# Optimization experiments

Measured on AMD Instinct MI355X. Metric: run time of the kernel, lower is better.

## Reference

```python
import jax, jax.numpy as jnp
import numpy as np
from jax.scipy.linalg import expm

S = 64          # alphabet size (codons)
M = 8           # number of models, prod(model_shape)
N_LEAVES = 32   # leaves of the balanced binary tree
N_EDGES = 62    # nodes 0..62, every non-root node has one parent edge (edge id == child node id)
B = 1024        # batch (alignment columns)
# per-level ranges of child-node ids; node 32+j has children (2j, 2j+1), etc.
LEVELS = [(0, 32), (32, 48), (48, 56), (56, 60), (60, 62)]


def inv_stereographic_projection(p):
    # maps R^{s-1} -> unit sphere S^{s-1}
    n2 = jnp.sum(p * p, axis=-1, keepdims=True)
    return jnp.concatenate([2.0 * p / (n2 + 1.0), (n2 - 1.0) / (n2 + 1.0)], axis=-1)


def generator(R, pi):
    # R: (M, s(s-1)/2) exchangeabilities, pi: (M, s) stationary distribution
    iu, ju = np.triu_indices(S, 1)
    A = jnp.zeros((M, S, S), R.dtype).at[:, iu, ju].set(R).at[:, ju, iu].set(R)
    Q = A * pi[:, None, :]                       # Q_ij = A_ij * pi_j (off-diagonal)
    row = jnp.sum(Q, axis=-1)                    # (M, S)
    return Q - jnp.eye(S, dtype=Q.dtype) * row[:, :, None]


def felsenstein(leave_configuration, R_inv, pi_inv, lengths):
    pi = inv_stereographic_projection(pi_inv) ** 2           # (M, S), rows sum to 1
    R = jnp.exp(R_inv)                                       # positive rates
    Q = generator(R, pi)                                     # (M, S, S)
    tQ = lengths[:, None, None, None] * Q[None]              # (E, M, S, S)
    P = jax.vmap(expm)(tQ.reshape(-1, S, S)).reshape(N_EDGES, M, S, S)
    # leaf alphas: tile leaf observations over the M models -> (n_leaves, B, M, S)
    prev = jnp.broadcast_to(
        leave_configuration.transpose(1, 0, 2)[:, :, None, :],
        (N_LEAVES, leave_configuration.shape[0], M, S))
    # level-synchronous pruning: messages up each parent edge, then product of the two children
    for a, b in LEVELS:
        msg = jnp.einsum('emcd,ebmd->ebmc', P[a:b], prev)    # per-edge transition
        prev = msg[0::2] * msg[1::2]                         # combine sibling pairs
    root = prev[0]                                           # (B, M, S)
    out = jnp.einsum('bms,ms->bm', root, pi)                 # P(data | model m)
    return out.reshape(out.shape[0], M)                      # (B, *model_shape)


def setup_inputs() -> dict:
    key = jax.random.key(0)
    k1, k2, k3, k4 = jax.random.split(key, 4)
    leave_configuration = jax.random.uniform(k1, (B, N_LEAVES, S), dtype=jnp.float32)
    tree_indices = jnp.zeros((B,), dtype=jnp.int32)          # single tree (F=1)
    R_inv = jax.random.uniform(k2, (M, S * (S - 1) // 2), dtype=jnp.float32,
                               minval=-1.0, maxval=1.0)
    pi_inv = jnp.full((M, S - 1), 1.0 / (np.sqrt(S) - 1.0), dtype=jnp.float32) \
        + 0.01 * jax.random.normal(k3, (M, S - 1), dtype=jnp.float32)
    lengths = jax.random.uniform(k4, (N_EDGES,), dtype=jnp.float32,
                                 minval=0.05, maxval=0.5)
    return {'leave_configuration': leave_configuration, 'R_inv': R_inv,
            'pi_inv': pi_inv, 'lengths': lengths, 'tree_indices': tree_indices}


def reference(leave_configuration, R_inv, pi_inv, lengths, tree_indices):
    # F=1: tf.dynamic_partition/gather_nd batch slicing is the identity, so
    # tree_indices is closed over / unused.
    return felsenstein(leave_configuration, R_inv, pi_inv, lengths)
```

## Files before the change

kernel.cpp:

```cpp
#include <hip/hip_runtime.h>

typedef unsigned short u16;
typedef unsigned int u32;
typedef __attribute__((ext_vector_type(8))) __bf16 bf16x8;
typedef __attribute__((ext_vector_type(4))) float f32x4;

constexpr size_t OFF_PI  = 0;
constexpr size_t OFF_PBH = 512;
constexpr size_t OFF_PBL = OFF_PBH + 1015808;

union FR { uint4 u; bf16x8 v; };

__device__ __forceinline__ void split_bf16(float x, u16& h, u16& l) {
  u32 b = __float_as_uint(x);
  u32 hb = (b + 0x7fffu + ((b >> 16) & 1u)) & 0xffff0000u;
  h = (u16)(hb >> 16);
  float r = x - __uint_as_float(hb);
  l = (u16)(__float_as_uint(r) >> 16);
}

__device__ __forceinline__ void split8(const f32x4 a, const f32x4 b,
                                       uint4& hi, uint4& lo) {
  u16 h[8], l[8];
  split_bf16(a.x, h[0], l[0]); split_bf16(a.y, h[1], l[1]);
  split_bf16(a.z, h[2], l[2]); split_bf16(a.w, h[3], l[3]);
  split_bf16(b.x, h[4], l[4]); split_bf16(b.y, h[5], l[5]);
  split_bf16(b.z, h[6], l[6]); split_bf16(b.w, h[7], l[7]);
  hi.x = h[0] | ((u32)h[1] << 16); hi.y = h[2] | ((u32)h[3] << 16);
  hi.z = h[4] | ((u32)h[5] << 16); hi.w = h[6] | ((u32)h[7] << 16);
  lo.x = l[0] | ((u32)l[1] << 16); lo.y = l[2] | ((u32)l[3] << 16);
  lo.z = l[4] | ((u32)l[5] << 16); lo.w = l[6] | ((u32)l[7] << 16);
}

__device__ __forceinline__ void mfma3(f32x4& a, const uint4 ah, const uint4 al,
                                      const uint4 bh, const uint4 bl) {
  FR Ah, Al, Bh, Bl;
  Ah.u = ah; Al.u = al; Bh.u = bh; Bl.u = bl;
  a = __builtin_amdgcn_mfma_f32_16x16x32_bf16(Ah.v, Bh.v, a, 0, 0, 0);
  a = __builtin_amdgcn_mfma_f32_16x16x32_bf16(Ah.v, Bl.v, a, 0, 0, 0);
  a = __builtin_amdgcn_mfma_f32_16x16x32_bf16(Al.v, Bh.v, a, 0, 0, 0);
}

__device__ __forceinline__ void xt_read2(const u32* b, int row, int chunk,
                                         uint4& hi, uint4& lo) {
  const int dw = (row << 5) + (((chunk + row) & 7) << 2);
  hi = *(const uint4*)&b[dw];
  lo = *(const uint4*)&b[2048 + dw];
}
__device__ __forceinline__ void xt_write4(u32* b, int row, int cp, int half,
                                          const f32x4 v) {
  u16 h[4], l[4];
  split_bf16(v.x, h[0], l[0]); split_bf16(v.y, h[1], l[1]);
  split_bf16(v.z, h[2], l[2]); split_bf16(v.w, h[3], l[3]);
  const int dw = (row << 5) + (((cp + row) & 7) << 2) + half * 2;
  uint2 hh, ll;
  hh.x = h[0] | ((u32)h[1] << 16); hh.y = h[2] | ((u32)h[3] << 16);
  ll.x = l[0] | ((u32)l[1] << 16); ll.y = l[2] | ((u32)l[3] << 16);
  *(uint2*)&b[dw] = hh;
  *(uint2*)&b[2048 + dw] = ll;
}

__global__ __launch_bounds__(512, 2) void k_pcomb(
    const float* __restrict__ R_inv, const float* __restrict__ pi_inv,
    const float* __restrict__ lengths, float* __restrict__ ws,
    u16* __restrict__ PBH, u16* __restrict__ PBL) {
  const int m = blockIdx.x & 7, prt = blockIdx.x >> 3;
  const int tid = threadIdx.x, lane = tid & 63, w = tid >> 6;
  const int ln = lane & 15, kq = lane >> 4;
  __shared__ float pis[64];
  __shared__ float n2s;
  __shared__ __align__(16) float Qs[64 * 68];
  __shared__ __align__(16) u32 PB[8][4096];

  if (tid < 64) {
    float p = (tid < 63) ? pi_inv[m * 63 + tid] : 0.f;
    float v = p * p;
    #pragma unroll
    for (int off = 32; off; off >>= 1) v += __shfl_down(v, off, 64);
    if (tid == 0) n2s = v;
  }
  __syncthreads();
  if (tid < 64) {
    const float den = n2s + 1.f;
    const float x = (tid < 63) ? 2.f * pi_inv[m * 63 + tid] / den
                               : (n2s - 1.f) / den;
    const float pv = x * x;
    pis[tid] = pv;
    if (prt == 0) ws[OFF_PI + (size_t)m * 64 + tid] = pv;
  }
  __syncthreads();
  for (int idx = tid; idx < 4096; idx += 512) {
    const int i = idx >> 6, j = idx & 63;
    float q = 0.f;
    if (i != j) {
      const int a = min(i, j), b = max(i, j);
      const int kk = a * (127 - a) / 2 + (b - a - 1);
      q = expf(R_inv[m * 2016 + kk]) * pis[j];
    }
    Qs[i * 68 + j] = q;
  }
  __syncthreads();
  if (tid < 64) {
    float s = 0.f;
    #pragma unroll 4
    for (int j4 = 0; j4 < 64; j4 += 4) {
      const f32x4 q = *(const f32x4*)&Qs[tid * 68 + j4];
      s += q.x + q.y + q.z + q.w;
    }
    Qs[tid * 68 + tid] = -s;
  }
  __syncthreads();

  float q[12][2][4];
  #pragma unroll
  for (int tt = 0; tt < 2; ++tt) {
    const int T = w + tt * 8, ct = T >> 2, bt = T & 3;
    #pragma unroll
    for (int r = 0; r < 4; ++r)
      q[0][tt][r] = Qs[(ct * 16 + kq * 4 + r) * 68 + bt * 16 + ln];
  }
  {
    const int i = tid >> 3, c = tid & 7;
    const f32x4 a = *(const f32x4*)&Qs[i * 68 + c * 8];
    const f32x4 b = *(const f32x4*)&Qs[i * 68 + c * 8 + 4];
    uint4 h, l;
    split8(a, b, h, l);
    const int dw = (i << 5) + (((c + i) & 7) << 2);
    *(uint4*)&PB[0][dw] = h;
    *(uint4*)&PB[0][2048 + dw] = l;
    const int j = i;
    f32x4 ca, cb;
    ca.x = Qs[(c * 8 + 0) * 68 + j]; ca.y = Qs[(c * 8 + 1) * 68 + j];
    ca.z = Qs[(c * 8 + 2) * 68 + j]; ca.w = Qs[(c * 8 + 3) * 68 + j];
    cb.x = Qs[(c * 8 + 4) * 68 + j]; cb.y = Qs[(c * 8 + 5) * 68 + j];
    cb.z = Qs[(c * 8 + 6) * 68 + j]; cb.w = Qs[(c * 8 + 7) * 68 + j];
    split8(ca, cb, h, l);
    *(uint4*)&PB[4][dw] = h;
    *(uint4*)&PB[4][2048 + dw] = l;
  }
  __syncthreads();

  const f32x4 z = {0.f, 0.f, 0.f, 0.f};
  auto tileP = [&](const u32* RX, const u32* CY, int T) -> f32x4 {
    const int ct = T >> 2, bt = T & 3;
    uint4 ah[2], al[2], bh[2], bl[2];
    #pragma unroll
    for (int kh = 0; kh < 2; ++kh) {
      xt_read2(RX, ct * 16 + ln, kh * 4 + kq, ah[kh], al[kh]);
      xt_read2(CY, bt * 16 + ln, kh * 4 + kq, bh[kh], bl[kh]);
    }
    f32x4 a = z;
    #pragma unroll
    for (int kh = 0; kh < 2; ++kh) mfma3(a, ah[kh], al[kh], bh[kh], bl[kh]);
    return a;
  };
  auto tileT = [&](const u32* RX, const u32* CY, int T) -> f32x4 {
    const int ct = T >> 2, bt = T & 3;
    uint4 ah[2], al[2], bh[2], bl[2];
    #pragma unroll
    for (int kh = 0; kh < 2; ++kh) {
      xt_read2(CY, ct * 16 + ln, kh * 4 + kq, ah[kh], al[kh]);
      xt_read2(RX, bt * 16 + ln, kh * 4 + kq, bh[kh], bl[kh]);
    }
    f32x4 a = z;
    #pragma unroll
    for (int kh = 0; kh < 2; ++kh) mfma3(a, ah[kh], al[kh], bh[kh], bl[kh]);
    return a;
  };
  auto wbuf = [&](u32* dst, int T, const f32x4 a) {
    const int ct = T >> 2, bt = T & 3;
    xt_write4(dst, bt * 16 + ln, 2 * ct + (kq >> 1), kq & 1, a);
  };

  #pragma unroll
  for (int tt = 0; tt < 2; ++tt) {
    const int T = w + tt * 8;
    const f32x4 a = tileP(PB[0], PB[4], T);
    #pragma unroll
    for (int r = 0; r < 4; ++r) q[1][tt][r] = a[r];
    wbuf(PB[5], T, a);
    wbuf(PB[1], T, tileT(PB[0], PB[4], T));
  }
  __syncthreads();
  #pragma unroll
  for (int tt = 0; tt < 2; ++tt) {
    const int T = w + tt * 8;
    const f32x4 a3 = tileP(PB[1], PB[4], T);
    const f32x4 a4 = tileP(PB[1], PB[5], T);
    #pragma unroll
    for (int r = 0; r < 4; ++r) { q[2][tt][r] = a3[r]; q[3][tt][r] = a4[r]; }
    wbuf(PB[6], T, a3);
    wbuf(PB[7], T, a4);
    wbuf(PB[2], T, tileT(PB[1], PB[5], T));
  }
  __syncthreads();
  #pragma unroll
  for (int tt = 0; tt < 2; ++tt) {
    const int T = w + tt * 8;
    const f32x4 a5 = tileP(PB[2], PB[4], T);
    const f32x4 a6 = tileP(PB[2], PB[5], T);
    const f32x4 a7 = tileP(PB[2], PB[6], T);
    const f32x4 a8 = tileP(PB[2], PB[7], T);
    #pragma unroll
    for (int r = 0; r < 4; ++r) {
      q[4][tt][r] = a5[r]; q[5][tt][r] = a6[r];
      q[6][tt][r] = a7[r]; q[7][tt][r] = a8[r];
    }
    wbuf(PB[3], T, tileT(PB[2], PB[7], T));
  }
  __syncthreads();
  #pragma unroll
  for (int tt = 0; tt < 2; ++tt) {
    const int T = w + tt * 8;
    const f32x4 a9  = tileP(PB[3], PB[4], T);
    const f32x4 a10 = tileP(PB[3], PB[5], T);
    const f32x4 a11 = tileP(PB[3], PB[6], T);
    const f32x4 a12 = tileP(PB[3], PB[7], T);
    #pragma unroll
    for (int r = 0; r < 4; ++r) {
      q[8][tt][r] = a9[r];  q[9][tt][r] = a10[r];
      q[10][tt][r] = a11[r]; q[11][tt][r] = a12[r];
    }
  }

  #pragma unroll
  for (int ei = 0; ei < 2; ++ei) {
    const int e = prt * 2 + ei;
    if (e >= 62) break;
    const float t = lengths[e];
    const size_t base = ((size_t)e * 8 + m) << 12;
    #pragma unroll
    for (int tt = 0; tt < 2; ++tt) {
      const int T = w + tt * 8, ct = T >> 2, bt = T & 3;
      float av[4];
      #pragma unroll
      for (int r = 0; r < 4; ++r)
        av[r] = (ct == bt && ln == kq * 4 + r) ? 1.f : 0.f;
      float cf = 1.f;
      #pragma unroll
      for (int k = 1; k <= 12; ++k) {
        cf *= t / (float)k;
        #pragma unroll
        for (int r = 0; r < 4; ++r) av[r] = fmaf(cf, q[k - 1][tt][r], av[r]);
      }
      #pragma unroll
      for (int r = 0; r < 4; ++r) {
        u16 h, l;
        split_bf16(av[r], h, l);
        const size_t off =
            base + (size_t)(ct * 16 + kq * 4 + r) * 64 + bt * 16 + ln;
        PBH[off] = h;
        PBL[off] = l;
      }
    }
  }
}

__global__ __launch_bounds__(512, 2) void k_tree(
    const float* __restrict__ leaves, const u16* __restrict__ Phi,
    const u16* __restrict__ Plo, const float* __restrict__ ws,
    float* __restrict__ out) {
  const int m = blockIdx.x & 7, btile = blockIdx.x >> 3;
  const int tid = threadIdx.x, lane = tid & 63, w = tid >> 6;
  const int ln = lane & 15, kq = lane >> 4;
  __shared__ __align__(16) u32 slots[16 * 2048];
  __shared__ float psum[2][4][16];
  const f32x4 z = {0.f, 0.f, 0.f, 0.f};

  auto node_read = [&](int slot, int row, int kh, uint4& bh, uint4& bl) {
    const int jc = kh * 8 + kq * 2;
    const u32* b = &slots[slot * 2048 + row * 64];
    const uint4 A = *(const uint4*)&b[((jc + row) & 15) << 2];
    const uint4 B = *(const uint4*)&b[((jc + 1 + row) & 15) << 2];
    bh.x = A.x; bh.y = A.y; bh.z = B.x; bh.w = B.y;
    bl.x = A.z; bl.y = A.w; bl.z = B.z; bl.w = B.w;
  };
  auto node_write = [&](int slot, int row, int jc, const f32x4 v) {
    u16 h[4], l[4];
    split_bf16(v.x, h[0], l[0]); split_bf16(v.y, h[1], l[1]);
    split_bf16(v.z, h[2], l[2]); split_bf16(v.w, h[3], l[3]);
    uint4 pk;
    pk.x = h[0] | ((u32)h[1] << 16); pk.y = h[2] | ((u32)h[3] << 16);
    pk.z = l[0] | ((u32)l[1] << 16); pk.w = l[2] | ((u32)l[3] << 16);
    *(uint4*)&slots[slot * 2048 + row * 64 + (((jc + row) & 15) << 2)] = pk;
  };

  auto do_pair = [&](int eb, int p, int s0, int s1, int outSlot, int bt0,
                     int nbt, int ct0, int nct, bool leaf, f32x4* rootout) {
    uint4 bfh[2][2][2], bfl[2][2][2];
    #pragma unroll
    for (int s = 0; s < 2; ++s)
      #pragma unroll
      for (int bi = 0; bi < 2; ++bi) {
        if (bi >= nbt) continue;
        const int row = (bt0 + bi) * 16 + ln;
        #pragma unroll
        for (int kh = 0; kh < 2; ++kh) {
          if (leaf) {
            const float* g = leaves + (size_t)(btile * 32 + row) * 2048 +
                             (size_t)(eb + 2 * p + s) * 64 + kh * 32 + kq * 8;
            const f32x4 xa = *(const f32x4*)g;
            const f32x4 xb = *(const f32x4*)(g + 4);
            split8(xa, xb, bfh[s][bi][kh], bfl[s][bi][kh]);
          } else {
            node_read(s ? s1 : s0, row, kh, bfh[s][bi][kh], bfl[s][bi][kh]);
          }
        }
      }
    uint4 ph[2][4][2], pl[2][4][2];
    #pragma unroll
    for (int s = 0; s < 2; ++s) {
      const size_t pb = ((size_t)(eb + 2 * p + s) * 8 + m) << 12;
      #pragma unroll
      for (int ci = 0; ci < 4; ++ci) {
        if (ci >= nct) continue;
        #pragma unroll
        for (int kh = 0; kh < 2; ++kh) {
          const size_t off =
              pb + (size_t)((ct0 + ci) * 16 + ln) * 64 + kh * 32 + kq * 8;
          ph[s][ci][kh] = *(const uint4*)(Phi + off);
          pl[s][ci][kh] = *(const uint4*)(Plo + off);
        }
      }
    }
    f32x4 a0[4][2];
    #pragma unroll
    for (int ci = 0; ci < 4; ++ci) {
      if (ci >= nct) continue;
      #pragma unroll
      for (int bi = 0; bi < 2; ++bi) {
        if (bi >= nbt) continue;
        f32x4 a = z;
        #pragma unroll
        for (int kh = 0; kh < 2; ++kh)
          mfma3(a, ph[0][ci][kh], pl[0][ci][kh], bfh[0][bi][kh], bfl[0][bi][kh]);
        a0[ci][bi] = a;
      }
    }
    #pragma unroll
    for (int ci = 0; ci < 4; ++ci) {
      if (ci >= nct) continue;
      #pragma unroll
      for (int bi = 0; bi < 2; ++bi) {
        if (bi >= nbt) continue;
        f32x4 a = z;
        #pragma unroll
        for (int kh = 0; kh < 2; ++kh)
          mfma3(a, ph[1][ci][kh], pl[1][ci][kh], bfh[1][bi][kh], bfl[1][bi][kh]);
        const f32x4 pr = a0[ci][bi] * a;
        if (rootout)
          *rootout = pr;
        else
          node_write(outSlot, (bt0 + bi) * 16 + ln, (ct0 + ci) * 4 + kq, pr);
      }
    }
  };

  do_pair(0, w, -1, -1, w, 0, 2, 0, 4, true, nullptr);
  do_pair(0, w + 8, -1, -1, w + 8, 0, 2, 0, 4, true, nullptr);
  __syncthreads();
  do_pair(32, w, 2 * w, 2 * w + 1, 2 * w, 0, 2, 0, 4, false, nullptr);
  __syncthreads();
  {
    const int j = w >> 1, bi = w & 1;
    do_pair(48, j, 4 * j, 4 * j + 2, 4 * j, bi, 1, 0, 4, false, nullptr);
  }
  __syncthreads();
  {
    const int j = w >> 2, bi = w & 1, ch = (w >> 1) & 1;
    do_pair(56, j, 8 * j, 8 * j + 4, 8 * j + 1, bi, 1, ch * 2, 2, false,
            nullptr);
  }
  __syncthreads();
  {
    f32x4 pr = z;
    do_pair(60, 0, 1, 9, -1, w & 1, 1, w >> 1, 1, false, &pr);
    const f32x4 piv =
        *(const f32x4*)&ws[OFF_PI + (size_t)m * 64 + (w >> 1) * 16 + kq * 4];
    float v = pr.x * piv.x + pr.y * piv.y + pr.z * piv.z + pr.w * piv.w;
    v += __shfl_xor(v, 16, 64);
    v += __shfl_xor(v, 32, 64);
    if (lane < 16) psum[w & 1][w >> 1][lane] = v;
  }
  __syncthreads();
  if (tid < 32) {
    const int bi = tid >> 4, bb = tid & 15;
    out[(size_t)(btile * 32 + tid) * 8 + m] =
        psum[bi][0][bb] + psum[bi][1][bb] + psum[bi][2][bb] + psum[bi][3][bb];
  }
}

extern "C" void kernel_launch(void* const* d_in, const int* in_sizes, int n_in,
                              void* d_out, int out_size, void* d_ws, size_t ws_size,
                              hipStream_t stream) {
  const float* leaves  = (const float*)d_in[0];
  const float* R_inv   = (const float*)d_in[1];
  const float* pi_inv  = (const float*)d_in[2];
  const float* lengths = (const float*)d_in[3];
  float* out = (float*)d_out;
  float* ws  = (float*)d_ws;

  u16* PBH = (u16*)(ws + OFF_PBH);
  u16* PBL = (u16*)(ws + OFF_PBL);

  hipLaunchKernelGGL(k_pcomb, dim3(256), dim3(512), 0, stream, R_inv, pi_inv,
                     lengths, ws, PBH, PBL);
  hipLaunchKernelGGL(k_tree, dim3(256), dim3(512), 0, stream, leaves, PBH, PBL,
                     ws, out);
}
```

Baseline: 119.8 us.

## Replace level-synchronous tree kernel with single-wave depth-first register recursion

The shared-memory, 8-wave level-synchronous pruning kernel is replaced by a template-recursive depth-first evaluation run by one 64-thread wave per (16-column tile, model). Intermediate node vectors stay in registers and are reshaped into MFMA B-operand layout with cross-lane shuffles instead of LDS round trips, which removes all __syncthreads and LDS traffic. The trade-off is a much smaller block size with only 512 single-wave blocks, heavier register pressure and code size from full unrolling, serial depth-first execution inside each wave, and P-matrix reloads per 16-column tile instead of per 32-column tile.

```diff
diff --git a/kernel.cpp b/kernel.cpp
--- a/kernel.cpp
+++ b/kernel.cpp
@@ -256,138 +256,140 @@
   }
 }
 
-__global__ __launch_bounds__(512, 2) void k_tree(
+struct NV { uint2 H[4]; uint2 L[4]; };
+
+struct Ctx {
+  const float* leaves;
+  const u16* Phi;
+  const u16* Plo;
+  int ln, kq, m;
+  size_t colbase;
+};
+
+__device__ __forceinline__ void leafB(const Ctx& c, int leaf, uint4 bh[2],
+                                      uint4 bl[2]) {
+  #pragma unroll
+  for (int kh = 0; kh < 2; ++kh) {
+    const float* g = c.leaves + (c.colbase + c.ln) * 2048 +
+                     (size_t)leaf * 64 + kh * 32 + c.kq * 8;
+    const f32x4 xa = *(const f32x4*)g;
+    const f32x4 xb = *(const f32x4*)(g + 4);
+    split8(xa, xb, bh[kh], bl[kh]);
+  }
+}
+
+__device__ __forceinline__ void nvB(const Ctx& c, const NV& v, uint4 bh[2],
+                                    uint4 bl[2]) {
+  const int A = c.ln + ((c.kq & 1) << 5);
+  const int B = A + 16;
+  const bool hiCt = (c.kq & 2) != 0;
+  #pragma unroll
+  for (int kh = 0; kh < 2; ++kh) {
+    const uint2 h0 = v.H[kh * 2], h1 = v.H[kh * 2 + 1];
+    const uint2 l0 = v.L[kh * 2], l1 = v.L[kh * 2 + 1];
+    const u32 hxA0 = __shfl((int)h0.x, A, 64), hyA0 = __shfl((int)h0.y, A, 64);
+    const u32 hxB0 = __shfl((int)h0.x, B, 64), hyB0 = __shfl((int)h0.y, B, 64);
+    const u32 hxA1 = __shfl((int)h1.x, A, 64), hyA1 = __shfl((int)h1.y, A, 64);
+    const u32 hxB1 = __shfl((int)h1.x, B, 64), hyB1 = __shfl((int)h1.y, B, 64);
+    bh[kh].x = hiCt ? hxA1 : hxA0; bh[kh].y = hiCt ? hyA1 : hyA0;
+    bh[kh].z = hiCt ? hxB1 : hxB0; bh[kh].w = hiCt ? hyB1 : hyB0;
+    const u32 lxA0 = __shfl((int)l0.x, A, 64), lyA0 = __shfl((int)l0.y, A, 64);
+    const u32 lxB0 = __shfl((int)l0.x, B, 64), lyB0 = __shfl((int)l0.y, B, 64);
+    const u32 lxA1 = __shfl((int)l1.x, A, 64), lyA1 = __shfl((int)l1.y, A, 64);
+    const u32 lxB1 = __shfl((int)l1.x, B, 64), lyB1 = __shfl((int)l1.y, B, 64);
+    bl[kh].x = hiCt ? lxA1 : lxA0; bl[kh].y = hiCt ? lyA1 : lyA0;
+    bl[kh].z = hiCt ? lxB1 : lxB0; bl[kh].w = hiCt ? lyB1 : lyB0;
+  }
+}
+
+__device__ __forceinline__ void edgeMsg(const Ctx& c, int e, const uint4 bh[2],
+                                        const uint4 bl[2], f32x4 mo[4]) {
+  const f32x4 z = {0.f, 0.f, 0.f, 0.f};
+  uint4 ph[4][2], pl[4][2];
+  const size_t pb = ((size_t)(e * 8 + c.m)) << 12;
+  #pragma unroll
+  for (int ci = 0; ci < 4; ++ci)
+    #pragma unroll
+    for (int kh = 0; kh < 2; ++kh) {
+      const size_t off = pb + (size_t)(ci * 16 + c.ln) * 64 + kh * 32 + c.kq * 8;
+      ph[ci][kh] = *(const uint4*)(c.Phi + off);
+      pl[ci][kh] = *(const uint4*)(c.Plo + off);
+    }
+  #pragma unroll
+  for (int ci = 0; ci < 4; ++ci) {
+    f32x4 a = z;
+    #pragma unroll
+    for (int kh = 0; kh < 2; ++kh)
+      mfma3(a, ph[ci][kh], pl[ci][kh], bh[kh], bl[kh]);
+    mo[ci] = a;
+  }
+}
+
+template <int N> __device__ __forceinline__ NV evalN(const Ctx& c);
+
+template <int C>
+__device__ __forceinline__ void childB(const Ctx& c, uint4 bh[2], uint4 bl[2]) {
+  if constexpr (C < 32) {
+    leafB(c, C, bh, bl);
+  } else {
+    const NV v = evalN<C>(c);
+    nvB(c, v, bh, bl);
+  }
+}
+
+template <int N>
+__device__ __forceinline__ NV evalN(const Ctx& c) {
+  constexpr int c0 = 2 * (N - 32);
+  uint4 b0h[2], b0l[2], b1h[2], b1l[2];
+  childB<c0>(c, b0h, b0l);
+  childB<c0 + 1>(c, b1h, b1l);
+  f32x4 m0[4], m1[4];
+  edgeMsg(c, c0, b0h, b0l, m0);
+  edgeMsg(c, c0 + 1, b1h, b1l, m1);
+  NV out;
+  #pragma unroll
+  for (int ci = 0; ci < 4; ++ci) {
+    const f32x4 pr = m0[ci] * m1[ci];
+    u16 h[4], l[4];
+    split_bf16(pr.x, h[0], l[0]); split_bf16(pr.y, h[1], l[1]);
+    split_bf16(pr.z, h[2], l[2]); split_bf16(pr.w, h[3], l[3]);
+    out.H[ci].x = h[0] | ((u32)h[1] << 16);
+    out.H[ci].y = h[2] | ((u32)h[3] << 16);
+    out.L[ci].x = l[0] | ((u32)l[1] << 16);
+    out.L[ci].y = l[2] | ((u32)l[3] << 16);
+  }
+  return out;
+}
+
+__global__ __launch_bounds__(64, 1) void k_treedf(
     const float* __restrict__ leaves, const u16* __restrict__ Phi,
     const u16* __restrict__ Plo, const float* __restrict__ ws,
     float* __restrict__ out) {
-  const int m = blockIdx.x & 7, btile = blockIdx.x >> 3;
-  const int tid = threadIdx.x, lane = tid & 63, w = tid >> 6;
-  const int ln = lane & 15, kq = lane >> 4;
-  __shared__ __align__(16) u32 slots[16 * 2048];
-  __shared__ float psum[2][4][16];
-  const f32x4 z = {0.f, 0.f, 0.f, 0.f};
-
-  auto node_read = [&](int slot, int row, int kh, uint4& bh, uint4& bl) {
-    const int jc = kh * 8 + kq * 2;
-    const u32* b = &slots[slot * 2048 + row * 64];
-    const uint4 A = *(const uint4*)&b[((jc + row) & 15) << 2];
-    const uint4 B = *(const uint4*)&b[((jc + 1 + row) & 15) << 2];
-    bh.x = A.x; bh.y = A.y; bh.z = B.x; bh.w = B.y;
-    bl.x = A.z; bl.y = A.w; bl.z = B.z; bl.w = B.w;
-  };
-  auto node_write = [&](int slot, int row, int jc, const f32x4 v) {
-    u16 h[4], l[4];
-    split_bf16(v.x, h[0], l[0]); split_bf16(v.y, h[1], l[1]);
-    split_bf16(v.z, h[2], l[2]); split_bf16(v.w, h[3], l[3]);
-    uint4 pk;
-    pk.x = h[0] | ((u32)h[1] << 16); pk.y = h[2] | ((u32)h[3] << 16);
-    pk.z = l[0] | ((u32)l[1] << 16); pk.w = l[2] | ((u32)l[3] << 16);
-    *(uint4*)&slots[slot * 2048 + row * 64 + (((jc + row) & 15) << 2)] = pk;
-  };
-
-  auto do_pair = [&](int eb, int p, int s0, int s1, int outSlot, int bt0,
-                     int nbt, int ct0, int nct, bool leaf, f32x4* rootout) {
-    uint4 bfh[2][2][2], bfl[2][2][2];
-    #pragma unroll
-    for (int s = 0; s < 2; ++s)
-      #pragma unroll
-      for (int bi = 0; bi < 2; ++bi) {
-        if (bi >= nbt) continue;
-        const int row = (bt0 + bi) * 16 + ln;
-        #pragma unroll
-        for (int kh = 0; kh < 2; ++kh) {
-          if (leaf) {
-            const float* g = leaves + (size_t)(btile * 32 + row) * 2048 +
-                             (size_t)(eb + 2 * p + s) * 64 + kh * 32 + kq * 8;
-            const f32x4 xa = *(const f32x4*)g;
-            const f32x4 xb = *(const f32x4*)(g + 4);
-            split8(xa, xb, bfh[s][bi][kh], bfl[s][bi][kh]);
-          } else {
-            node_read(s ? s1 : s0, row, kh, bfh[s][bi][kh], bfl[s][bi][kh]);
-          }
-        }
-      }
-    uint4 ph[2][4][2], pl[2][4][2];
-    #pragma unroll
-    for (int s = 0; s < 2; ++s) {
-      const size_t pb = ((size_t)(eb + 2 * p + s) * 8 + m) << 12;
-      #pragma unroll
-      for (int ci = 0; ci < 4; ++ci) {
-        if (ci >= nct) continue;
-        #pragma unroll
-        for (int kh = 0; kh < 2; ++kh) {
-          const size_t off =
-              pb + (size_t)((ct0 + ci) * 16 + ln) * 64 + kh * 32 + kq * 8;
-          ph[s][ci][kh] = *(const uint4*)(Phi + off);
-          pl[s][ci][kh] = *(const uint4*)(Plo + off);
-        }
-      }
-    }
-    f32x4 a0[4][2];
-    #pragma unroll
-    for (int ci = 0; ci < 4; ++ci) {
-      if (ci >= nct) continue;
-      #pragma unroll
-      for (int bi = 0; bi < 2; ++bi) {
-        if (bi >= nbt) continue;
-        f32x4 a = z;
-        #pragma unroll
-        for (int kh = 0; kh < 2; ++kh)
-          mfma3(a, ph[0][ci][kh], pl[0][ci][kh], bfh[0][bi][kh], bfl[0][bi][kh]);
-        a0[ci][bi] = a;
-      }
-    }
-    #pragma unroll
-    for (int ci = 0; ci < 4; ++ci) {
-      if (ci >= nct) continue;
-      #pragma unroll
-      for (int bi = 0; bi < 2; ++bi) {
-        if (bi >= nbt) continue;
-        f32x4 a = z;
-        #pragma unroll
-        for (int kh = 0; kh < 2; ++kh)
-          mfma3(a, ph[1][ci][kh], pl[1][ci][kh], bfh[1][bi][kh], bfl[1][bi][kh]);
-        const f32x4 pr = a0[ci][bi] * a;
-        if (rootout)
-          *rootout = pr;
-        else
-          node_write(outSlot, (bt0 + bi) * 16 + ln, (ct0 + ci) * 4 + kq, pr);
-      }
-    }
-  };
-
-  do_pair(0, w, -1, -1, w, 0, 2, 0, 4, true, nullptr);
-  do_pair(0, w + 8, -1, -1, w + 8, 0, 2, 0, 4, true, nullptr);
-  __syncthreads();
-  do_pair(32, w, 2 * w, 2 * w + 1, 2 * w, 0, 2, 0, 4, false, nullptr);
-  __syncthreads();
-  {
-    const int j = w >> 1, bi = w & 1;
-    do_pair(48, j, 4 * j, 4 * j + 2, 4 * j, bi, 1, 0, 4, false, nullptr);
-  }
-  __syncthreads();
-  {
-    const int j = w >> 2, bi = w & 1, ch = (w >> 1) & 1;
-    do_pair(56, j, 8 * j, 8 * j + 4, 8 * j + 1, bi, 1, ch * 2, 2, false,
-            nullptr);
-  }
-  __syncthreads();
-  {
-    f32x4 pr = z;
-    do_pair(60, 0, 1, 9, -1, w & 1, 1, w >> 1, 1, false, &pr);
+  const int m = blockIdx.x & 7, ctile = blockIdx.x >> 3;
+  const int lane = threadIdx.x & 63;
+  Ctx c;
+  c.leaves = leaves; c.Phi = Phi; c.Plo = Plo;
+  c.ln = lane & 15; c.kq = lane >> 4; c.m = m;
+  c.colbase = (size_t)ctile * 16;
+
+  uint4 b0h[2], b0l[2], b1h[2], b1l[2];
+  childB<60>(c, b0h, b0l);
+  childB<61>(c, b1h, b1l);
+  f32x4 m0[4], m1[4];
+  edgeMsg(c, 60, b0h, b0l, m0);
+  edgeMsg(c, 61, b1h, b1l, m1);
+
+  float v = 0.f;
+  #pragma unroll
+  for (int ci = 0; ci < 4; ++ci) {
+    const f32x4 pr = m0[ci] * m1[ci];
     const f32x4 piv =
-        *(const f32x4*)&ws[OFF_PI + (size_t)m * 64 + (w >> 1) * 16 + kq * 4];
-    float v = pr.x * piv.x + pr.y * piv.y + pr.z * piv.z + pr.w * piv.w;
-    v += __shfl_xor(v, 16, 64);
-    v += __shfl_xor(v, 32, 64);
-    if (lane < 16) psum[w & 1][w >> 1][lane] = v;
-  }
-  __syncthreads();
-  if (tid < 32) {
-    const int bi = tid >> 4, bb = tid & 15;
-    out[(size_t)(btile * 32 + tid) * 8 + m] =
-        psum[bi][0][bb] + psum[bi][1][bb] + psum[bi][2][bb] + psum[bi][3][bb];
-  }
+        *(const f32x4*)&ws[OFF_PI + (size_t)m * 64 + ci * 16 + c.kq * 4];
+    v += pr.x * piv.x + pr.y * piv.y + pr.z * piv.z + pr.w * piv.w;
+  }
+  v += __shfl_xor(v, 16, 64);
+  v += __shfl_xor(v, 32, 64);
+  if (lane < 16) out[(c.colbase + c.ln) * 8 + m] = v;
 }
 
 extern "C" void kernel_launch(void* const* d_in, const int* in_sizes, int n_in,
@@ -405,6 +407,6 @@
 
   hipLaunchKernelGGL(k_pcomb, dim3(256), dim3(512), 0, stream, R_inv, pi_inv,
                      lengths, ws, PBH, PBL);
-  hipLaunchKernelGGL(k_tree, dim3(256), dim3(512), 0, stream, leaves, PBH, PBL,
+  hipLaunchKernelGGL(k_treedf, dim3(512), dim3(64), 0, stream, leaves, PBH, PBL,
                      ws, out);
 }
```

Measured after the change: 283.8 us. 137% more time.

## Split tree kernel into two launches to raise block parallelism for lower levels

Applied to the files above, without the earlier changes.

Splits the tree pruning into k_treeA, which handles the leaves through level 2 across 1024 blocks (four subtrees per batch tile and model) and writes the level-2 node messages to workspace, and k_treeB, which finishes the top two levels and the root reduction. This is meant to fill the GPU with more blocks during the heavy leaf levels, with smaller shared memory per block, instead of 256 blocks each walking the whole tree. In exchange it adds a global-memory round trip for the intermediate messages and an extra kernel launch. It falls back to the old single kernel if the workspace is too small.

```diff
diff --git a/kernel.cpp b/kernel.cpp
--- a/kernel.cpp
+++ b/kernel.cpp
@@ -8,6 +8,8 @@
 constexpr size_t OFF_PI  = 0;
 constexpr size_t OFF_PBH = 512;
 constexpr size_t OFF_PBL = OFF_PBH + 1015808;
+constexpr size_t OFF_NB2 = OFF_PBL + 1015808;
+constexpr size_t NB2_FLOATS = 2097152;
 
 union FR { uint4 u; bf16x8 v; };
 
@@ -58,6 +60,21 @@
   ll.x = l[0] | ((u32)l[1] << 16); ll.y = l[2] | ((u32)l[3] << 16);
   *(uint2*)&b[dw] = hh;
   *(uint2*)&b[2048 + dw] = ll;
+}
+
+__device__ __forceinline__ uint4 pack_hl(const f32x4 v) {
+  u16 h[4], l[4];
+  split_bf16(v.x, h[0], l[0]); split_bf16(v.y, h[1], l[1]);
+  split_bf16(v.z, h[2], l[2]); split_bf16(v.w, h[3], l[3]);
+  uint4 pk;
+  pk.x = h[0] | ((u32)h[1] << 16); pk.y = h[2] | ((u32)h[3] << 16);
+  pk.z = l[0] | ((u32)l[1] << 16); pk.w = l[2] | ((u32)l[3] << 16);
+  return pk;
+}
+__device__ __forceinline__ void unpack_hl(const uint4 A, const uint4 B,
+                                          uint4& bh, uint4& bl) {
+  bh.x = A.x; bh.y = A.y; bh.z = B.x; bh.w = B.y;
+  bl.x = A.z; bl.y = A.w; bl.z = B.z; bl.w = B.w;
 }
 
 __global__ __launch_bounds__(512, 2) void k_pcomb(
@@ -272,17 +289,11 @@
     const u32* b = &slots[slot * 2048 + row * 64];
     const uint4 A = *(const uint4*)&b[((jc + row) & 15) << 2];
     const uint4 B = *(const uint4*)&b[((jc + 1 + row) & 15) << 2];
-    bh.x = A.x; bh.y = A.y; bh.z = B.x; bh.w = B.y;
-    bl.x = A.z; bl.y = A.w; bl.z = B.z; bl.w = B.w;
+    unpack_hl(A, B, bh, bl);
   };
   auto node_write = [&](int slot, int row, int jc, const f32x4 v) {
-    u16 h[4], l[4];
-    split_bf16(v.x, h[0], l[0]); split_bf16(v.y, h[1], l[1]);
-    split_bf16(v.z, h[2], l[2]); split_bf16(v.w, h[3], l[3]);
-    uint4 pk;
-    pk.x = h[0] | ((u32)h[1] << 16); pk.y = h[2] | ((u32)h[3] << 16);
-    pk.z = l[0] | ((u32)l[1] << 16); pk.w = l[2] | ((u32)l[3] << 16);
-    *(uint4*)&slots[slot * 2048 + row * 64 + (((jc + row) & 15) << 2)] = pk;
+    *(uint4*)&slots[slot * 2048 + row * 64 + (((jc + row) & 15) << 2)] =
+        pack_hl(v);
   };
 
   auto do_pair = [&](int eb, int p, int s0, int s1, int outSlot, int bt0,
@@ -390,6 +401,217 @@
   }
 }
 
+__global__ __launch_bounds__(512, 2) void k_treeA(
+    const float* __restrict__ leaves, const u16* __restrict__ Phi,
+    const u16* __restrict__ Plo, float* __restrict__ ws) {
+  const int m = blockIdx.x & 7;
+  const int q = (blockIdx.x >> 3) & 3;
+  const int btile = blockIdx.x >> 5;
+  const int tid = threadIdx.x, lane = tid & 63, w = tid >> 6;
+  const int ln = lane & 15, kq = lane >> 4;
+  __shared__ __align__(16) u32 slots[6 * 2048];
+  uint4* NB2 = (uint4*)(ws + OFF_NB2);
+  const f32x4 z = {0.f, 0.f, 0.f, 0.f};
+
+  auto slot_read = [&](int slot, int row, int kh, uint4& bh, uint4& bl) {
+    const int jc = kh * 8 + kq * 2;
+    const u32* b = &slots[slot * 2048 + row * 64];
+    const uint4 A = *(const uint4*)&b[((jc + row) & 15) << 2];
+    const uint4 B = *(const uint4*)&b[((jc + 1 + row) & 15) << 2];
+    unpack_hl(A, B, bh, bl);
+  };
+  auto slot_write = [&](int slot, int row, int jc, const f32x4 v) {
+    *(uint4*)&slots[slot * 2048 + row * 64 + (((jc + row) & 15) << 2)] =
+        pack_hl(v);
+  };
+  auto nb2_write = [&](int nidx, int row, int jc, const f32x4 v) {
+    NB2[(((size_t)(nidx * 8 + m) * 32 + btile) * 32 + row) * 16 +
+        ((jc + row) & 15)] = pack_hl(v);
+  };
+  auto edge_msg = [&](int e, const uint4 bh[2], const uint4 bl[2], int ct0,
+                      int nct, f32x4* mo) {
+    const size_t pb = ((size_t)(e * 8 + m)) << 12;
+    uint4 ph[4][2], pl[4][2];
+    #pragma unroll
+    for (int ci = 0; ci < 4; ++ci) {
+      if (ci >= nct) continue;
+      #pragma unroll
+      for (int kh = 0; kh < 2; ++kh) {
+        const size_t off =
+            pb + (size_t)((ct0 + ci) * 16 + ln) * 64 + kh * 32 + kq * 8;
+        ph[ci][kh] = *(const uint4*)(Phi + off);
+        pl[ci][kh] = *(const uint4*)(Plo + off);
+      }
+    }
+    #pragma unroll
+    for (int ci = 0; ci < 4; ++ci) {
+      if (ci >= nct) continue;
+      f32x4 a = z;
+      #pragma unroll
+      for (int kh = 0; kh < 2; ++kh)
+        mfma3(a, ph[ci][kh], pl[ci][kh], bh[kh], bl[kh]);
+      mo[ci] = a;
+    }
+  };
+
+  {
+    const int ch = w & 1, p = w >> 1;
+    const int row = ch * 16 + ln;
+    const int e0 = 8 * q + 2 * p, e1 = e0 + 1;
+    uint4 bh[2][2], bl[2][2];
+    #pragma unroll
+    for (int s = 0; s < 2; ++s)
+      #pragma unroll
+      for (int kh = 0; kh < 2; ++kh) {
+        const float* g = leaves + (size_t)(btile * 32 + row) * 2048 +
+                         (size_t)(s ? e1 : e0) * 64 + kh * 32 + kq * 8;
+        split8(*(const f32x4*)g, *(const f32x4*)(g + 4), bh[s][kh], bl[s][kh]);
+      }
+    f32x4 m0[4], m1[4];
+    edge_msg(e0, bh[0], bl[0], 0, 4, m0);
+    edge_msg(e1, bh[1], bl[1], 0, 4, m1);
+    #pragma unroll
+    for (int ci = 0; ci < 4; ++ci)
+      slot_write(p, row, ci * 4 + kq, m0[ci] * m1[ci]);
+  }
+  __syncthreads();
+  {
+    const int r = w >> 2, ch = (w >> 1) & 1, q2 = w & 1;
+    const int row = ch * 16 + ln, ct0 = 2 * q2;
+    const int e0 = 32 + 4 * q + 2 * r, e1 = e0 + 1;
+    uint4 bh[2][2], bl[2][2];
+    #pragma unroll
+    for (int s = 0; s < 2; ++s)
+      #pragma unroll
+      for (int kh = 0; kh < 2; ++kh)
+        slot_read(2 * r + s, row, kh, bh[s][kh], bl[s][kh]);
+    f32x4 m0[4], m1[4];
+    edge_msg(e0, bh[0], bl[0], ct0, 2, m0);
+    edge_msg(e1, bh[1], bl[1], ct0, 2, m1);
+    #pragma unroll
+    for (int ci = 0; ci < 2; ++ci)
+      slot_write(4 + r, row, (ct0 + ci) * 4 + kq, m0[ci] * m1[ci]);
+  }
+  __syncthreads();
+  {
+    const int ch = w & 1, cq = w >> 1;
+    const int row = ch * 16 + ln;
+    const int e0 = 48 + 2 * q, e1 = e0 + 1;
+    uint4 bh[2][2], bl[2][2];
+    #pragma unroll
+    for (int s = 0; s < 2; ++s)
+      #pragma unroll
+      for (int kh = 0; kh < 2; ++kh)
+        slot_read(4 + s, row, kh, bh[s][kh], bl[s][kh]);
+    f32x4 m0[4], m1[4];
+    edge_msg(e0, bh[0], bl[0], cq, 1, m0);
+    edge_msg(e1, bh[1], bl[1], cq, 1, m1);
+    nb2_write(q, row, cq * 4 + kq, m0[0] * m1[0]);
+  }
+}
+
+__global__ __launch_bounds__(512, 2) void k_treeB(
+    const u16* __restrict__ Phi, const u16* __restrict__ Plo,
+    const float* __restrict__ ws, float* __restrict__ out) {
+  const int m = blockIdx.x & 7, btile = blockIdx.x >> 3;
+  const int tid = threadIdx.x, lane = tid & 63, w = tid >> 6;
+  const int ln = lane & 15, kq = lane >> 4;
+  __shared__ __align__(16) u32 slots[2 * 2048];
+  __shared__ float psum[2][4][16];
+  const uint4* NB2 = (const uint4*)(ws + OFF_NB2);
+  const f32x4 z = {0.f, 0.f, 0.f, 0.f};
+
+  auto slot_read = [&](int slot, int row, int kh, uint4& bh, uint4& bl) {
+    const int jc = kh * 8 + kq * 2;
+    const u32* b = &slots[slot * 2048 + row * 64];
+    const uint4 A = *(const uint4*)&b[((jc + row) & 15) << 2];
+    const uint4 B = *(const uint4*)&b[((jc + 1 + row) & 15) << 2];
+    unpack_hl(A, B, bh, bl);
+  };
+  auto slot_write = [&](int slot, int row, int jc, const f32x4 v) {
+    *(uint4*)&slots[slot * 2048 + row * 64 + (((jc + row) & 15) << 2)] =
+        pack_hl(v);
+  };
+  auto nb2_read = [&](int nidx, int row, int kh, uint4& bh, uint4& bl) {
+    const int jc = kh * 8 + kq * 2;
+    const uint4* b =
+        NB2 + (((size_t)(nidx * 8 + m) * 32 + btile) * 32 + row) * 16;
+    const uint4 A = b[(jc + row) & 15];
+    const uint4 B = b[(jc + 1 + row) & 15];
+    unpack_hl(A, B, bh, bl);
+  };
+  auto edge_msg = [&](int e, const uint4 bh[2], const uint4 bl[2], int ct0,
+                      int nct, f32x4* mo) {
+    const size_t pb = ((size_t)(e * 8 + m)) << 12;
+    uint4 ph[4][2], pl[4][2];
+    #pragma unroll
+    for (int ci = 0; ci < 4; ++ci) {
+      if (ci >= nct) continue;
+      #pragma unroll
+      for (int kh = 0; kh < 2; ++kh) {
+        const size_t off =
+            pb + (size_t)((ct0 + ci) * 16 + ln) * 64 + kh * 32 + kq * 8;
+        ph[ci][kh] = *(const uint4*)(Phi + off);
+        pl[ci][kh] = *(const uint4*)(Plo + off);
+      }
+    }
+    #pragma unroll
+    for (int ci = 0; ci < 4; ++ci) {
+      if (ci >= nct) continue;
+      f32x4 a = z;
+      #pragma unroll
+      for (int kh = 0; kh < 2; ++kh)
+        mfma3(a, ph[ci][kh], pl[ci][kh], bh[kh], bl[kh]);
+      mo[ci] = a;
+    }
+  };
+
+  {
+    const int r = w >> 2, ch = (w >> 1) & 1, q2 = w & 1;
+    const int row = ch * 16 + ln, ct0 = 2 * q2;
+    const int e0 = 56 + 2 * r, e1 = e0 + 1;
+    uint4 bh[2][2], bl[2][2];
+    #pragma unroll
+    for (int s = 0; s < 2; ++s)
+      #pragma unroll
+      for (int kh = 0; kh < 2; ++kh)
+        nb2_read(2 * r + s, row, kh, bh[s][kh], bl[s][kh]);
+    f32x4 m0[4], m1[4];
+    edge_msg(e0, bh[0], bl[0], ct0, 2, m0);
+    edge_msg(e1, bh[1], bl[1], ct0, 2, m1);
+    #pragma unroll
+    for (int ci = 0; ci < 2; ++ci)
+      slot_write(r, row, (ct0 + ci) * 4 + kq, m0[ci] * m1[ci]);
+  }
+  __syncthreads();
+  {
+    const int ch = w & 1, cq = w >> 1;
+    const int row = ch * 16 + ln;
+    uint4 bh[2][2], bl[2][2];
+    #pragma unroll
+    for (int s = 0; s < 2; ++s)
+      #pragma unroll
+      for (int kh = 0; kh < 2; ++kh)
+        slot_read(s, row, kh, bh[s][kh], bl[s][kh]);
+    f32x4 m0[4], m1[4];
+    edge_msg(60, bh[0], bl[0], cq, 1, m0);
+    edge_msg(61, bh[1], bl[1], cq, 1, m1);
+    const f32x4 pr = m0[0] * m1[0];
+    const f32x4 piv =
+        *(const f32x4*)&ws[OFF_PI + (size_t)m * 64 + cq * 16 + kq * 4];
+    float v = pr.x * piv.x + pr.y * piv.y + pr.z * piv.z + pr.w * piv.w;
+    v += __shfl_xor(v, 16, 64);
+    v += __shfl_xor(v, 32, 64);
+    if (lane < 16) psum[ch][cq][lane] = v;
+  }
+  __syncthreads();
+  if (tid < 32) {
+    const int ch = tid >> 4, bb = tid & 15;
+    out[(size_t)(btile * 32 + tid) * 8 + m] =
+        psum[ch][0][bb] + psum[ch][1][bb] + psum[ch][2][bb] + psum[ch][3][bb];
+  }
+}
+
 extern "C" void kernel_launch(void* const* d_in, const int* in_sizes, int n_in,
                               void* d_out, int out_size, void* d_ws, size_t ws_size,
                               hipStream_t stream) {
@@ -405,6 +627,15 @@
 
   hipLaunchKernelGGL(k_pcomb, dim3(256), dim3(512), 0, stream, R_inv, pi_inv,
                      lengths, ws, PBH, PBL);
-  hipLaunchKernelGGL(k_tree, dim3(256), dim3(512), 0, stream, leaves, PBH, PBL,
-                     ws, out);
-}
+
+  const bool big_ws = ws_size >= (OFF_NB2 + NB2_FLOATS) * sizeof(float);
+  if (big_ws) {
+    hipLaunchKernelGGL(k_treeA, dim3(1024), dim3(512), 0, stream, leaves, PBH,
+                       PBL, ws);
+    hipLaunchKernelGGL(k_treeB, dim3(256), dim3(512), 0, stream, PBH, PBL, ws,
+                       out);
+  } else {
+    hipLaunchKernelGGL(k_tree, dim3(256), dim3(512), 0, stream, leaves, PBH,
+                       PBL, ws, out);
+  }
+}
```

After: 145.7 us. +21.7%, slower.
